# Performance work log

Hardware: AMD Instinct MI355X
Metric: run time of the kernel (lower is better)

## Reference

```python
import jax, jax.numpy as jnp
import numpy as np

HEADS = 16
DIM_HEAD = 64
SCALE = DIM_HEAD ** -0.5
LN_EPS = 1e-5


def setup_inputs() -> dict:
    key = jax.random.key(0)
    k1, k2, k3 = jax.random.split(key, 3)
    b, s, d = 2, 2048, 1024
    inner = HEADS * DIM_HEAD
    x = jax.random.normal(k1, (b, s, d), dtype=jnp.float32)
    w_qkv = jax.random.normal(k2, (d, 3 * inner), dtype=jnp.float32) * (d ** -0.5)
    w_out = jax.random.normal(k3, (inner, d), dtype=jnp.float32) * (inner ** -0.5)
    return {
        "x": x,
        "ln_gamma": jnp.ones((d,), jnp.float32),
        "ln_beta": jnp.zeros((d,), jnp.float32),
        "w_qkv": w_qkv,
        "w_out": w_out,
        "b_out": jnp.zeros((d,), jnp.float32),
    }


def _layernorm(x, gamma, beta):
    mu = jnp.mean(x, axis=-1, keepdims=True)
    var = jnp.var(x, axis=-1, keepdims=True)
    return (x - mu) * jax.lax.rsqrt(var + LN_EPS) * gamma + beta


def reference(x, ln_gamma, ln_beta, w_qkv, w_out, b_out):
    b, s, d = x.shape
    xn = _layernorm(x, ln_gamma, ln_beta)
    qkv = xn @ w_qkv                       # [b, s, 3*inner]
    q, k, v = jnp.split(qkv, 3, axis=-1)
    def heads(t):
        return t.reshape(b, s, HEADS, DIM_HEAD).transpose(0, 2, 1, 3)  # [b, h, s, dh]
    q, k, v = heads(q), heads(k), heads(v)
    dots = jnp.einsum("bhqd,bhkd->bhqk", q, k) * SCALE   # [b, h, s, s]
    attn = jax.nn.softmax(dots, axis=-1)
    out = jnp.einsum("bhqk,bhkd->bhqd", attn, v)          # [b, h, s, dh]
    out = out.transpose(0, 2, 1, 3).reshape(b, s, HEADS * DIM_HEAD)
    return out @ w_out + b_out
```

## Files before the change

kernel.cpp:

```cpp
#include <hip/hip_runtime.h>
#include <hip/hip_bf16.h>
#include <stdint.h>

#define NH     16
#define DHEAD  64
#define SEQ    2048
#define DMODEL 1024
#define NBATCH 2
#define INNER  1024
#define QKVN   3072
#define ROWS   4096
#define ATT_QB 64
#define ATT_KB 64

typedef __attribute__((ext_vector_type(8))) __bf16 bf16x8;
typedef __attribute__((ext_vector_type(4))) float floatx4;
typedef __attribute__((ext_vector_type(16))) float floatx16;

__device__ __forceinline__ unsigned short f2bf(float f) {
    union { __bf16 b; unsigned short u; } c; c.b = (__bf16)f; return c.u;
}

__device__ __forceinline__ unsigned int pk2(float lo, float hi) {
    union { ushort2 s; unsigned int u; } c;
    c.s.x = f2bf(lo); c.s.y = f2bf(hi); return c.u;
}

__device__ __forceinline__ float fexp2(float x) {
#if __has_builtin(__builtin_amdgcn_exp2f)
    return __builtin_amdgcn_exp2f(x);
#else
    float r; asm("v_exp_f32 %0, %1" : "=v"(r) : "v"(x)); return r;
#endif
}

typedef __attribute__((address_space(1))) void gvoid;
typedef __attribute__((address_space(3))) void lvoid;
__device__ __forceinline__ void gl_lds16(const void* g, void* l) {
    __builtin_amdgcn_global_load_lds((gvoid*)g, (lvoid*)l, 16, 0, 0);
}

__global__ __launch_bounds__(256) void transpose_f2b(
        const float* __restrict__ in, unsigned short* __restrict__ out,
        int rows, int cols) {
    __shared__ unsigned short tile[32][33];
    const int bx = blockIdx.x * 32, by = blockIdx.y * 32;
    const int tx = threadIdx.x & 31, ty = threadIdx.x >> 5;
    for (int i = ty; i < 32; i += 8)
        tile[i][tx] = f2bf(in[(size_t)(by + i) * cols + bx + tx]);
    __syncthreads();
    for (int i = ty; i < 32; i += 8)
        out[(size_t)(bx + i) * rows + by + tx] = tile[tx][i];
}

__global__ __launch_bounds__(256) void ln_kernel(
        const float* __restrict__ x,
        const float* __restrict__ gamma,
        const float* __restrict__ beta,
        unsigned short* __restrict__ xn) {
    __shared__ float red[4][2];
    const int row = blockIdx.x, t = threadIdx.x;
    const size_t base = (size_t)row * DMODEL + t * 4;
    float4 v = *(const float4*)(x + base);
    float s  = v.x + v.y + v.z + v.w;
    float ss = v.x*v.x + v.y*v.y + v.z*v.z + v.w*v.w;
    for (int off = 32; off >= 1; off >>= 1) {
        s  += __shfl_xor(s,  off);
        ss += __shfl_xor(ss, off);
    }
    const int w = t >> 6, lane = t & 63;
    if (lane == 0) { red[w][0] = s; red[w][1] = ss; }
    __syncthreads();
    if (t == 0) {
        float S  = red[0][0] + red[1][0] + red[2][0] + red[3][0];
        float SS = red[0][1] + red[1][1] + red[2][1] + red[3][1];
        float mu  = S * (1.f / DMODEL);
        float var = SS * (1.f / DMODEL) - mu * mu;
        red[0][0] = mu; red[0][1] = rsqrtf(var + 1e-5f);
    }
    __syncthreads();
    const float mu = red[0][0], rstd = red[0][1];
    float4 g = *(const float4*)(gamma + t * 4);
    float4 bb = *(const float4*)(beta + t * 4);
    ushort4 o;
    o.x = f2bf((v.x - mu) * rstd * g.x + bb.x);
    o.y = f2bf((v.y - mu) * rstd * g.y + bb.y);
    o.z = f2bf((v.z - mu) * rstd * g.z + bb.z);
    o.w = f2bf((v.w - mu) * rstd * g.w + bb.w);
    *(ushort4*)(xn + base) = o;
}

__global__ __launch_bounds__(256) void gemm_qkv(
        const unsigned short* __restrict__ A,
        const unsigned short* __restrict__ Bt,
        unsigned short* __restrict__ qP,
        unsigned short* __restrict__ kP,
        unsigned short* __restrict__ vT) {
    const int K = DMODEL;
    __shared__ __align__(16) unsigned short sA[128 * 32];
    __shared__ __align__(16) unsigned short sB[128 * 32];
    __shared__ __align__(16) unsigned short tb[2][64 * 72];
    const int t = threadIdx.x;
    const int mBase = blockIdx.y * 128, nBase = blockIdx.x * 128;
    const int w = t >> 6, lane = t & 63, quad = lane >> 4, l16 = lane & 15;
    const int wm = (w >> 1) * 64, wn = (w & 1) * 64;
    const int srow = t >> 2, sch = t & 3;
    floatx4 acc[4][4];
    for (int mi = 0; mi < 4; mi++)
        for (int ni = 0; ni < 4; ni++) acc[mi][ni] = (floatx4)0.f;

    for (int k0 = 0; k0 < K; k0 += 32) {
        #pragma unroll
        for (int c = 0; c < 2; c++) {
            const int row = c * 64 + srow;
            const int gcol = (sch ^ ((row >> 1) & 3)) * 8;
            gl_lds16(&A[(size_t)(mBase + row) * K + k0 + gcol], &sA[(c * 256 + w * 64) * 8]);
            gl_lds16(&Bt[(size_t)(nBase + row) * K + k0 + gcol], &sB[(c * 256 + w * 64) * 8]);
        }
        __syncthreads();
        bf16x8 af[4], bfv[4];
        #pragma unroll
        for (int mi = 0; mi < 4; mi++) {
            const int r = wm + mi * 16 + l16;
            af[mi] = *(const bf16x8*)&sA[r * 32 + (quad ^ ((r >> 1) & 3)) * 8];
        }
        #pragma unroll
        for (int ni = 0; ni < 4; ni++) {
            const int r = wn + ni * 16 + l16;
            bfv[ni] = *(const bf16x8*)&sB[r * 32 + (quad ^ ((r >> 1) & 3)) * 8];
        }
        #pragma unroll
        for (int mi = 0; mi < 4; mi++)
            #pragma unroll
            for (int ni = 0; ni < 4; ni++)
                acc[mi][ni] = __builtin_amdgcn_mfma_f32_16x16x32_bf16(
                    af[mi], bfv[ni], acc[mi][ni], 0, 0, 0);
        __syncthreads();
    }
    const int reg = nBase >> 10;
    if (reg == 2) {
        #pragma unroll
        for (int ni = 0; ni < 4; ni++) {
            const int col = nBase + wn + ni * 16 + l16;
            const int h = (col & 1023) >> 6, dh = col & 63;
            #pragma unroll
            for (int mi = 0; mi < 4; mi++) {
                const int row0 = mBase + wm + mi * 16 + quad * 4;
                const int b = row0 >> 11, s0 = row0 & 2047;
                ushort4 o;
                o.x = f2bf(acc[mi][ni][0]); o.y = f2bf(acc[mi][ni][1]);
                o.z = f2bf(acc[mi][ni][2]); o.w = f2bf(acc[mi][ni][3]);
                *(ushort4*)&vT[((size_t)(b * NH + h) * DHEAD + dh) * SEQ + s0] = o;
            }
        }
    } else {
        unsigned short* dst = (reg == 0) ? qP : kP;
        const float scl = (reg == 0) ? 0.18033688011112042f : 1.f;
        const int hh = ((nBase + wn) & 1023) >> 6;
        #pragma unroll
        for (int ph = 0; ph < 2; ph++) {
            if ((w >> 1) == ph) {
                unsigned short* tb_ = &tb[w & 1][0];
                #pragma unroll
                for (int mi = 0; mi < 4; mi++)
                    #pragma unroll
                    for (int ni = 0; ni < 4; ni++)
                        #pragma unroll
                        for (int i = 0; i < 4; i++)
                            tb_[(mi * 16 + quad * 4 + i) * 72 + ni * 16 + l16] =
                                f2bf(acc[mi][ni][i] * scl);
                asm volatile("s_waitcnt lgkmcnt(0)" ::: "memory");
                const int row_g = mBase + wm + lane;
                const int b = row_g >> 11, sr = row_g & 2047;
                unsigned short* orow = dst + ((size_t)(b * NH + hh) * SEQ + sr) * DHEAD;
                #pragma unroll
                for (int c = 0; c < 8; c++)
                    *(bf16x8*)&orow[c * 8] = *(const bf16x8*)&tb_[lane * 72 + c * 8];
            }
            __syncthreads();
        }
    }
}

__global__ __launch_bounds__(256) void gemm_out(
        const unsigned short* __restrict__ A,
        const unsigned short* __restrict__ Bt,
        float* __restrict__ C,
        const int M, const int N, const int K,
        const float* __restrict__ bias) {
    __shared__ __align__(16) unsigned short sA[128 * 32];
    __shared__ __align__(16) unsigned short sB[64 * 32];
    const int t = threadIdx.x;
    const int mBase = blockIdx.y * 128, nBase = blockIdx.x * 64;
    const int w = t >> 6, lane = t & 63, quad = lane >> 4, l16 = lane & 15;
    const int wm = (w >> 1) * 64, wn = (w & 1) * 32;
    const int srow = t >> 2, sch = t & 3;
    floatx4 acc[4][2];
    for (int mi = 0; mi < 4; mi++)
        for (int ni = 0; ni < 2; ni++) acc[mi][ni] = (floatx4)0.f;

    for (int k0 = 0; k0 < K; k0 += 32) {
        #pragma unroll
        for (int c = 0; c < 2; c++) {
            const int row = c * 64 + srow;
            const int gcol = (sch ^ ((row >> 1) & 3)) * 8;
            gl_lds16(&A[(size_t)(mBase + row) * K + k0 + gcol], &sA[(c * 256 + w * 64) * 8]);
        }
        {
            const int gcol = (sch ^ ((srow >> 1) & 3)) * 8;
            gl_lds16(&Bt[(size_t)(nBase + srow) * K + k0 + gcol], &sB[(w * 64) * 8]);
        }
        __syncthreads();
        bf16x8 af[4], bfv[2];
        #pragma unroll
        for (int mi = 0; mi < 4; mi++) {
            const int r = wm + mi * 16 + l16;
            af[mi] = *(const bf16x8*)&sA[r * 32 + (quad ^ ((r >> 1) & 3)) * 8];
        }
        #pragma unroll
        for (int ni = 0; ni < 2; ni++) {
            const int r = wn + ni * 16 + l16;
            bfv[ni] = *(const bf16x8*)&sB[r * 32 + (quad ^ ((r >> 1) & 3)) * 8];
        }
        #pragma unroll
        for (int mi = 0; mi < 4; mi++)
            #pragma unroll
            for (int ni = 0; ni < 2; ni++)
                acc[mi][ni] = __builtin_amdgcn_mfma_f32_16x16x32_bf16(
                    af[mi], bfv[ni], acc[mi][ni], 0, 0, 0);
        __syncthreads();
    }
    #pragma unroll
    for (int mi = 0; mi < 4; mi++)
        #pragma unroll
        for (int ni = 0; ni < 2; ni++) {
            const int col = nBase + wn + ni * 16 + l16;
            const float badd = bias ? bias[col] : 0.f;
            #pragma unroll
            for (int i = 0; i < 4; i++) {
                const int row = mBase + wm + mi * 16 + quad * 4 + i;
                C[(size_t)row * N + col] = acc[mi][ni][i] + badd;
            }
        }
}

__global__ __launch_bounds__(128, 2) void attn_kernel(
        const unsigned short* __restrict__ qP,
        const unsigned short* __restrict__ kP,
        const unsigned short* __restrict__ vT,
        unsigned short* __restrict__ aout) {
    __shared__ __align__(16) unsigned short sK[2][ATT_KB * 64];
    __shared__ __align__(16) unsigned short sV[2][ATT_KB * 64];
    const int t = threadIdx.x, w = t >> 6, lane = t & 63;
    const int l32 = lane & 31, half = lane >> 5;
    const int bid = blockIdx.x;
    const int xcd = bid & 7, slot = bid >> 3;
    const int bh = xcd * 4 + (slot >> 5);
    const int qb = slot & 31;
    const int b = bh >> 4, h = bh & 15;
    const int qbase = qb * ATT_QB + w * 32;

    bf16x8 qf[4];
    #pragma unroll
    for (int kd = 0; kd < 4; kd++)
        qf[kd] = *(const bf16x8*)&qP[
            ((size_t)bh * SEQ + qbase + l32) * DHEAD + kd * 16 + half * 8];

    floatx16 oac[2];
    oac[0] = (floatx16)0.f; oac[1] = (floatx16)0.f;
    float lS = 0.f;

    const unsigned short* kb = kP + (size_t)bh * SEQ * DHEAD;
    const unsigned short* vb = vT + (size_t)bh * DHEAD * SEQ;
    const int r8 = lane >> 3, sw8 = ((lane & 7) ^ r8) * 8;

    auto stage = [&](int it, int bi) {
        const int kv0 = it * ATT_KB;
        #pragma unroll
        for (int ii = 0; ii < 4; ii++) {
            const int row = w * 32 + ii * 8 + r8;
            gl_lds16(kb + (size_t)(kv0 + row) * DHEAD + sw8,
                     (void*)&sK[bi][(w * 32 + ii * 8) * 64]);
            gl_lds16(vb + (size_t)row * SEQ + kv0 + sw8,
                     (void*)&sV[bi][(w * 32 + ii * 8) * 64]);
        }
    };
    stage(0, 0);

    const int NIT = SEQ / ATT_KB;
    for (int it = 0; it < NIT; ++it) {
        __syncthreads();
        const int bi = it & 1;
        bf16x8 kf[2][4];
        #pragma unroll
        for (int tt = 0; tt < 2; tt++)
            #pragma unroll
            for (int kd = 0; kd < 4; kd++)
                kf[tt][kd] = *(const bf16x8*)&sK[bi][(tt * 32 + l32) * 64 +
                                                    8 * ((half + 2 * kd) ^ (l32 & 7))];
        if (it + 1 < NIT) stage(it + 1, bi ^ 1);
        bf16x8 vf[2][4];
        #pragma unroll
        for (int dt = 0; dt < 2; dt++)
            #pragma unroll
            for (int kd = 0; kd < 4; kd++)
                vf[dt][kd] = *(const bf16x8*)&sV[bi][(dt * 32 + l32) * 64 +
                                                    8 * ((half + 2 * kd) ^ (l32 & 7))];

        floatx16 sv0 = (floatx16)0.f, sv1 = (floatx16)0.f;
        __builtin_amdgcn_s_setprio(1);
        #pragma unroll
        for (int kd = 0; kd < 4; kd++)
            sv0 = __builtin_amdgcn_mfma_f32_32x32x16_bf16(kf[0][kd], qf[kd], sv0, 0, 0, 0);
        #pragma unroll
        for (int kd = 0; kd < 4; kd++)
            sv1 = __builtin_amdgcn_mfma_f32_32x32x16_bf16(kf[1][kd], qf[kd], sv1, 0, 0, 0);
        __builtin_amdgcn_s_setprio(0);

        float p[32];
        #pragma unroll
        for (int i = 0; i < 16; i++) p[i]      = fexp2(sv0[i]);
        #pragma unroll
        for (int i = 0; i < 16; i++) p[16 + i] = fexp2(sv1[i]);
        {
            float s0 = 0.f, s1 = 0.f;
            #pragma unroll
            for (int i = 0; i < 16; i++) { s0 += p[i]; s1 += p[16 + i]; }
            float s = s0 + s1;
            s += __shfl_xor(s, 32);
            lS += s;
        }

        bf16x8 pf[4];
        #pragma unroll
        for (int tt = 0; tt < 2; tt++)
            #pragma unroll
            for (int e = 0; e < 2; e++) {
                const int base = tt * 16 + e * 8;
                unsigned int c01 = pk2(p[base + 0], p[base + 1]);
                unsigned int c23 = pk2(p[base + 2], p[base + 3]);
                unsigned int c45 = pk2(p[base + 4], p[base + 5]);
                unsigned int c67 = pk2(p[base + 6], p[base + 7]);
                asm("v_permlane32_swap_b32 %0, %1" : "+v"(c01), "+v"(c45));
                asm("v_permlane32_swap_b32 %0, %1" : "+v"(c23), "+v"(c67));
                union { unsigned int u[4]; bf16x8 v; } fr;
                fr.u[0] = c01; fr.u[1] = c23; fr.u[2] = c45; fr.u[3] = c67;
                pf[tt * 2 + e] = fr.v;
            }

        __builtin_amdgcn_s_setprio(1);
        #pragma unroll
        for (int kd = 0; kd < 4; kd++)
            oac[0] = __builtin_amdgcn_mfma_f32_32x32x16_bf16(vf[0][kd], pf[kd], oac[0], 0, 0, 0);
        #pragma unroll
        for (int kd = 0; kd < 4; kd++)
            oac[1] = __builtin_amdgcn_mfma_f32_32x32x16_bf16(vf[1][kd], pf[kd], oac[1], 0, 0, 0);
        __builtin_amdgcn_s_setprio(0);
    }

    const float rl = 1.f / lS;
    unsigned short* orow = aout + ((size_t)(b * SEQ + qbase + l32)) * INNER + h * DHEAD;
    #pragma unroll
    for (int dt = 0; dt < 2; dt++)
        #pragma unroll
        for (int g = 0; g < 4; g++) {
            ushort4 o;
            o.x = f2bf(oac[dt][g * 4 + 0] * rl);
            o.y = f2bf(oac[dt][g * 4 + 1] * rl);
            o.z = f2bf(oac[dt][g * 4 + 2] * rl);
            o.w = f2bf(oac[dt][g * 4 + 3] * rl);
            *(ushort4*)&orow[dt * 32 + g * 8 + half * 4] = o;
        }
}

extern "C" void kernel_launch(void* const* d_in, const int* in_sizes, int n_in,
                              void* d_out, int out_size, void* d_ws, size_t ws_size,
                              hipStream_t stream) {
    const float* x     = (const float*)d_in[0];
    const float* gamma = (const float*)d_in[1];
    const float* beta  = (const float*)d_in[2];
    const float* wqkv  = (const float*)d_in[3];
    const float* wout  = (const float*)d_in[4];
    const float* bout  = (const float*)d_in[5];
    float* out = (float*)d_out;

    unsigned short* ws     = (unsigned short*)d_ws;
    unsigned short* xn     = ws;
    unsigned short* wqkvT  = xn     + (size_t)ROWS * DMODEL;
    unsigned short* qPb    = wqkvT  + (size_t)QKVN * DMODEL;
    unsigned short* kPb    = qPb    + (size_t)NBATCH * NH * SEQ * DHEAD;
    unsigned short* vTb    = kPb    + (size_t)NBATCH * NH * SEQ * DHEAD;
    unsigned short* attnO  = vTb    + (size_t)NBATCH * NH * SEQ * DHEAD;
    unsigned short* woutT  = attnO  + (size_t)ROWS * INNER;

    transpose_f2b<<<dim3(QKVN / 32, DMODEL / 32), 256, 0, stream>>>(wqkv, wqkvT, DMODEL, QKVN);
    transpose_f2b<<<dim3(DMODEL / 32, INNER / 32), 256, 0, stream>>>(wout, woutT, INNER, DMODEL);
    ln_kernel<<<ROWS, 256, 0, stream>>>(x, gamma, beta, xn);
    gemm_qkv<<<dim3(QKVN / 128, ROWS / 128), 256, 0, stream>>>(xn, wqkvT, qPb, kPb, vTb);
    attn_kernel<<<dim3((SEQ / ATT_QB) * NBATCH * NH), 128, 0, stream>>>(
        qPb, kPb, vTb, attnO);
    gemm_out<<<dim3(DMODEL / 64, ROWS / 128), 256, 0, stream>>>(
        attnO, woutT, out, ROWS, DMODEL, INNER, bout);
}
```

Measured before the change: 214.7 us.

## Split attention KV tiles across two wave pairs with LDS reduction

The attention block grows from 2 to 4 waves. Each pair of waves handles half of every 64-key tile for the same 32 query rows, so per-wave MFMA and exp work per iteration is halved. Partial outputs and row sums are combined through LDS at the end. The intent is more waves in flight to hide latency, at the cost of a final reduction, extra syncs and more register and occupancy pressure from launch bounds of 4 blocks per CU. Softmax uses no running max, so the two partial results can simply be added.

```diff
diff --git a/kernel.cpp b/kernel.cpp
--- a/kernel.cpp
+++ b/kernel.cpp
@@ -244,7 +244,7 @@
         }
 }
 
-__global__ __launch_bounds__(128, 2) void attn_kernel(
+__global__ __launch_bounds__(256, 4) void attn_kernel(
         const unsigned short* __restrict__ qP,
         const unsigned short* __restrict__ kP,
         const unsigned short* __restrict__ vT,
@@ -253,12 +253,13 @@
     __shared__ __align__(16) unsigned short sV[2][ATT_KB * 64];
     const int t = threadIdx.x, w = t >> 6, lane = t & 63;
     const int l32 = lane & 31, half = lane >> 5;
+    const int qh = w & 1, kh = w >> 1;
     const int bid = blockIdx.x;
     const int xcd = bid & 7, slot = bid >> 3;
     const int bh = xcd * 4 + (slot >> 5);
     const int qb = slot & 31;
     const int b = bh >> 4, h = bh & 15;
-    const int qbase = qb * ATT_QB + w * 32;
+    const int qbase = qb * ATT_QB + qh * 32;
 
     bf16x8 qf[4];
     #pragma unroll
@@ -277,12 +278,12 @@
     auto stage = [&](int it, int bi) {
         const int kv0 = it * ATT_KB;
         #pragma unroll
-        for (int ii = 0; ii < 4; ii++) {
-            const int row = w * 32 + ii * 8 + r8;
+        for (int ii = 0; ii < 2; ii++) {
+            const int row = w * 16 + ii * 8 + r8;
             gl_lds16(kb + (size_t)(kv0 + row) * DHEAD + sw8,
-                     (void*)&sK[bi][(w * 32 + ii * 8) * 64]);
+                     (void*)&sK[bi][(w * 16 + ii * 8) * 64]);
             gl_lds16(vb + (size_t)row * SEQ + kv0 + sw8,
-                     (void*)&sV[bi][(w * 32 + ii * 8) * 64]);
+                     (void*)&sV[bi][(w * 16 + ii * 8) * 64]);
         }
     };
     stage(0, 0);
@@ -291,86 +292,104 @@
     for (int it = 0; it < NIT; ++it) {
         __syncthreads();
         const int bi = it & 1;
-        bf16x8 kf[2][4];
-        #pragma unroll
-        for (int tt = 0; tt < 2; tt++)
-            #pragma unroll
-            for (int kd = 0; kd < 4; kd++)
-                kf[tt][kd] = *(const bf16x8*)&sK[bi][(tt * 32 + l32) * 64 +
-                                                    8 * ((half + 2 * kd) ^ (l32 & 7))];
         if (it + 1 < NIT) stage(it + 1, bi ^ 1);
-        bf16x8 vf[2][4];
-        #pragma unroll
-        for (int dt = 0; dt < 2; dt++)
-            #pragma unroll
-            for (int kd = 0; kd < 4; kd++)
-                vf[dt][kd] = *(const bf16x8*)&sV[bi][(dt * 32 + l32) * 64 +
-                                                    8 * ((half + 2 * kd) ^ (l32 & 7))];
-
-        floatx16 sv0 = (floatx16)0.f, sv1 = (floatx16)0.f;
+
+        bf16x8 kf[4];
+        #pragma unroll
+        for (int kd = 0; kd < 4; kd++) {
+            const int r = kh * 32 + l32;
+            kf[kd] = *(const bf16x8*)&sK[bi][r * 64 + 8 * ((2 * kd + half) ^ (l32 & 7))];
+        }
+
+        floatx16 sv = (floatx16)0.f;
         __builtin_amdgcn_s_setprio(1);
         #pragma unroll
         for (int kd = 0; kd < 4; kd++)
-            sv0 = __builtin_amdgcn_mfma_f32_32x32x16_bf16(kf[0][kd], qf[kd], sv0, 0, 0, 0);
-        #pragma unroll
-        for (int kd = 0; kd < 4; kd++)
-            sv1 = __builtin_amdgcn_mfma_f32_32x32x16_bf16(kf[1][kd], qf[kd], sv1, 0, 0, 0);
+            sv = __builtin_amdgcn_mfma_f32_32x32x16_bf16(kf[kd], qf[kd], sv, 0, 0, 0);
         __builtin_amdgcn_s_setprio(0);
 
-        float p[32];
-        #pragma unroll
-        for (int i = 0; i < 16; i++) p[i]      = fexp2(sv0[i]);
-        #pragma unroll
-        for (int i = 0; i < 16; i++) p[16 + i] = fexp2(sv1[i]);
+        float p[16];
+        #pragma unroll
+        for (int i = 0; i < 16; i++) p[i] = fexp2(sv[i]);
         {
-            float s0 = 0.f, s1 = 0.f;
-            #pragma unroll
-            for (int i = 0; i < 16; i++) { s0 += p[i]; s1 += p[16 + i]; }
-            float s = s0 + s1;
+            float s = 0.f;
+            #pragma unroll
+            for (int i = 0; i < 16; i++) s += p[i];
             s += __shfl_xor(s, 32);
             lS += s;
         }
 
-        bf16x8 pf[4];
-        #pragma unroll
-        for (int tt = 0; tt < 2; tt++)
-            #pragma unroll
-            for (int e = 0; e < 2; e++) {
-                const int base = tt * 16 + e * 8;
-                unsigned int c01 = pk2(p[base + 0], p[base + 1]);
-                unsigned int c23 = pk2(p[base + 2], p[base + 3]);
-                unsigned int c45 = pk2(p[base + 4], p[base + 5]);
-                unsigned int c67 = pk2(p[base + 6], p[base + 7]);
-                asm("v_permlane32_swap_b32 %0, %1" : "+v"(c01), "+v"(c45));
-                asm("v_permlane32_swap_b32 %0, %1" : "+v"(c23), "+v"(c67));
-                union { unsigned int u[4]; bf16x8 v; } fr;
-                fr.u[0] = c01; fr.u[1] = c23; fr.u[2] = c45; fr.u[3] = c67;
-                pf[tt * 2 + e] = fr.v;
-            }
+        bf16x8 pf[2];
+        #pragma unroll
+        for (int kd = 0; kd < 2; kd++) {
+            const int base = kd * 8;
+            unsigned int c01 = pk2(p[base + 0], p[base + 1]);
+            unsigned int c23 = pk2(p[base + 2], p[base + 3]);
+            unsigned int c45 = pk2(p[base + 4], p[base + 5]);
+            unsigned int c67 = pk2(p[base + 6], p[base + 7]);
+            asm("v_permlane32_swap_b32 %0, %1" : "+v"(c01), "+v"(c45));
+            asm("v_permlane32_swap_b32 %0, %1" : "+v"(c23), "+v"(c67));
+            union { unsigned int u[4]; bf16x8 v; } fr;
+            fr.u[0] = c01; fr.u[1] = c23; fr.u[2] = c45; fr.u[3] = c67;
+            pf[kd] = fr.v;
+        }
 
         __builtin_amdgcn_s_setprio(1);
         #pragma unroll
-        for (int kd = 0; kd < 4; kd++)
-            oac[0] = __builtin_amdgcn_mfma_f32_32x32x16_bf16(vf[0][kd], pf[kd], oac[0], 0, 0, 0);
-        #pragma unroll
-        for (int kd = 0; kd < 4; kd++)
-            oac[1] = __builtin_amdgcn_mfma_f32_32x32x16_bf16(vf[1][kd], pf[kd], oac[1], 0, 0, 0);
+        for (int dt = 0; dt < 2; dt++)
+            #pragma unroll
+            for (int kd = 0; kd < 2; kd++) {
+                const int r = dt * 32 + l32;
+                bf16x8 vf = *(const bf16x8*)&sV[bi][
+                    r * 64 + 8 * ((kh * 4 + kd * 2 + half) ^ (l32 & 7))];
+                oac[dt] = __builtin_amdgcn_mfma_f32_32x32x16_bf16(vf, pf[kd], oac[dt], 0, 0, 0);
+            }
         __builtin_amdgcn_s_setprio(0);
     }
 
-    const float rl = 1.f / lS;
-    unsigned short* orow = aout + ((size_t)(b * SEQ + qbase + l32)) * INNER + h * DHEAD;
-    #pragma unroll
-    for (int dt = 0; dt < 2; dt++)
-        #pragma unroll
-        for (int g = 0; g < 4; g++) {
-            ushort4 o;
-            o.x = f2bf(oac[dt][g * 4 + 0] * rl);
-            o.y = f2bf(oac[dt][g * 4 + 1] * rl);
-            o.z = f2bf(oac[dt][g * 4 + 2] * rl);
-            o.w = f2bf(oac[dt][g * 4 + 3] * rl);
-            *(ushort4*)&orow[dt * 32 + g * 8 + half * 4] = o;
-        }
+    __syncthreads();
+    float* redO = (float*)&sK[0][0];
+    float* redL = (float*)&sV[0][0];
+    if (kh == 1) {
+        #pragma unroll
+        for (int dt = 0; dt < 2; dt++)
+            #pragma unroll
+            for (int g = 0; g < 4; g++) {
+                const int c = dt * 4 + g;
+                float4 o4;
+                o4.x = oac[dt][g * 4 + 0]; o4.y = oac[dt][g * 4 + 1];
+                o4.z = oac[dt][g * 4 + 2]; o4.w = oac[dt][g * 4 + 3];
+                *(float4*)&redO[((size_t)qh * 64 + lane) * 32 + 4 * (c ^ (lane & 7))] = o4;
+            }
+        if (half == 0) redL[qh * 32 + l32] = lS;
+    }
+    __syncthreads();
+    if (kh == 0) {
+        #pragma unroll
+        for (int dt = 0; dt < 2; dt++)
+            #pragma unroll
+            for (int g = 0; g < 4; g++) {
+                const int c = dt * 4 + g;
+                float4 o4 = *(const float4*)&redO[
+                    ((size_t)qh * 64 + lane) * 32 + 4 * (c ^ (lane & 7))];
+                oac[dt][g * 4 + 0] += o4.x; oac[dt][g * 4 + 1] += o4.y;
+                oac[dt][g * 4 + 2] += o4.z; oac[dt][g * 4 + 3] += o4.w;
+            }
+        lS += redL[qh * 32 + l32];
+        const float rl = 1.f / lS;
+        unsigned short* orow = aout + ((size_t)(b * SEQ + qbase + l32)) * INNER + h * DHEAD;
+        #pragma unroll
+        for (int dt = 0; dt < 2; dt++)
+            #pragma unroll
+            for (int g = 0; g < 4; g++) {
+                ushort4 o;
+                o.x = f2bf(oac[dt][g * 4 + 0] * rl);
+                o.y = f2bf(oac[dt][g * 4 + 1] * rl);
+                o.z = f2bf(oac[dt][g * 4 + 2] * rl);
+                o.w = f2bf(oac[dt][g * 4 + 3] * rl);
+                *(ushort4*)&orow[dt * 32 + g * 8 + half * 4] = o;
+            }
+    }
 }
 
 extern "C" void kernel_launch(void* const* d_in, const int* in_sizes, int n_in,
@@ -397,7 +416,7 @@
     transpose_f2b<<<dim3(DMODEL / 32, INNER / 32), 256, 0, stream>>>(wout, woutT, INNER, DMODEL);
     ln_kernel<<<ROWS, 256, 0, stream>>>(x, gamma, beta, xn);
     gemm_qkv<<<dim3(QKVN / 128, ROWS / 128), 256, 0, stream>>>(xn, wqkvT, qPb, kPb, vTb);
-    attn_kernel<<<dim3((SEQ / ATT_QB) * NBATCH * NH), 128, 0, stream>>>(
+    attn_kernel<<<dim3((SEQ / ATT_QB) * NBATCH * NH), 256, 0, stream>>>(
         qPb, kPb, vTb, attnO);
     gemm_out<<<dim3(DMODEL / 64, ROWS / 128), 256, 0, stream>>>(
         attnO, woutT, out, ROWS, DMODEL, INNER, bout);
```

Result: no change. 213.1 us (-0.8%).
